# Performance work log

Hardware: AMD Instinct MI355X
Metric: run time of the kernel (lower is better)

## Reference

```python
import jax, jax.numpy as jnp
import numpy as np

NSAMPLE = 32
RADIUS = 5.0
EPS = 1e-5  # BatchNorm eps (torch default)


def setup_inputs() -> dict:
    key = jax.random.key(0)
    ks = jax.random.split(key, 8)
    B, N, C = 4, 4096, 64
    mlp = [64, 64, 64]
    inp = {
        "pos1": jax.random.normal(ks[0], (B, 3, N), jnp.float32),
        "pos2": jax.random.normal(ks[1], (B, 3, N), jnp.float32),
        "feature1": jax.random.normal(ks[2], (B, C, N), jnp.float32),
        "feature2": jax.random.normal(ks[3], (B, C, N), jnp.float32),
    }
    last = 2 * C + 3  # concat corr: feat2 + feat1 + xyz-diff
    for i, oc in enumerate(mlp):
        inp[f"W{i}"] = jax.random.normal(ks[4 + i], (oc, last), jnp.float32) / np.float32(np.sqrt(last))
        inp[f"g{i}"] = jnp.ones((oc,), jnp.float32)
        inp[f"b{i}"] = jnp.zeros((oc,), jnp.float32)
        last = oc
    return inp


def _group(f, idx):
    # f: (B, C, M), idx: (B, N, S) -> (B, C, N, S)
    return jax.vmap(lambda fb, ib: fb[:, ib])(f, idx)


def _bn_relu(x, g, b):
    # training-mode BatchNorm2d over (B, N, S) per channel, then ReLU
    m = x.mean(axis=(0, 2, 3), keepdims=True)
    v = x.var(axis=(0, 2, 3), keepdims=True)
    y = g[None, :, None, None] * (x - m) * jax.lax.rsqrt(v + EPS) + b[None, :, None, None]
    return jax.nn.relu(y)


def _forward(pos1, pos2, feature1, feature2, params):
    B, _, N = pos1.shape
    p1t = pos1.transpose(0, 2, 1)  # (B, N, 3)
    p2t = pos2.transpose(0, 2, 1)  # (B, M, 3)
    # squared pairwise distances (B, N, M)
    sq = (jnp.sum(p1t * p1t, -1, keepdims=True)
          - 2.0 * jnp.einsum('bnc,bmc->bnm', p1t, p2t)
          + jnp.sum(p2t * p2t, -1)[:, None, :])
    neg, idx = jax.lax.top_k(-sq, NSAMPLE)  # ascending-distance KNN
    dist = jnp.sqrt(jnp.maximum(-neg, 0.0))
    # replace out-of-radius neighbors with the nearest neighbor index
    idx = jnp.where(dist > RADIUS, idx[:, :, :1], idx)
    pos2_g = _group(pos2, idx)                       # (B, 3, N, S)
    pos_diff = pos2_g - pos1[:, :, :, None]
    feat2_g = _group(feature2, idx)                  # (B, C, N, S)
    feat1_rep = jnp.broadcast_to(feature1[:, :, :, None],
                                 (B, feature1.shape[1], N, NSAMPLE))
    x = jnp.concatenate([pos_diff, feat2_g, feat1_rep], axis=1)  # (B, 2C+3, N, S)
    for W, g, b in params:
        x = jnp.einsum('oc,bcns->bons', W, x)  # 1x1 conv, no bias
        x = _bn_relu(x, g, b)
    return x.max(axis=-1)  # max-pool over neighbors -> (B, mlp[-1], N)


def reference(pos1, pos2, feature1, feature2, W0, g0, b0, W1, g1, b1, W2, g2, b2):
    params = [(W0, g0, b0), (W1, g1, b1), (W2, g2, b2)]
    feat1_new = _forward(pos1, pos2, feature1, feature2, params)
    return (pos1, feat1_new)
```

## Files before the change

kernel.cpp:

```cpp
#include <hip/hip_runtime.h>
#include <hip/hip_bf16.h>


#define N_ 4096
#define S_ 32
#define PTOT 524288.0f

typedef unsigned short u16;
typedef unsigned int   u32;
typedef unsigned long long u64;
typedef __attribute__((ext_vector_type(8))) short short8;
typedef __attribute__((ext_vector_type(4))) float f32x4;

__device__ __forceinline__ float b2f(u16 u){
  union { u32 i; float f; } x; x.i = ((u32)u) << 16; return x.f;
}
__device__ __forceinline__ u16 f2b(float f){
  __hip_bfloat16 h = __float2bfloat16(f);
  return *(u16*)&h;
}
__device__ __forceinline__ u32 fenc(float f){
  u32 u = __float_as_uint(f);
  return (u & 0x80000000u) ? ~u : (u | 0x80000000u);
}
__device__ __forceinline__ float fdec(u32 k){
  return __uint_as_float((k & 0x80000000u) ? (k & 0x7FFFFFFFu) : ~k);
}
__device__ __forceinline__ int TIX(int r, int c){ return (r << 6) + (c ^ ((r & 7) << 3)); }
#define MFMA16(a,b,c) __builtin_amdgcn_mfma_f32_16x16x32_bf16((a),(b),(c),0,0,0)

__global__ void k_copy(const uint4* __restrict__ s, uint4* __restrict__ d){
  int i = blockIdx.x * 256 + threadIdx.x;
  d[i] = s[i];
}

#define PLCNT(T, OUT) { int _c = 0;                                           \
  _Pragma("unroll")                                                           \
  for (int _it = 0; _it < 64; ++_it) _c += (dl[_it] < (T)) ? 1 : 0;           \
  _Pragma("unroll")                                                           \
  for (int _d = 1; _d < 64; _d <<= 1) _c += __shfl_xor(_c, _d);               \
  OUT = (u32)_c; }

__global__ __launch_bounds__(256) void k_knn(const float* __restrict__ pos1,
        const float* __restrict__ pos2, int* __restrict__ idxb){
  __shared__ u64 lkey[4][96];
  int b = blockIdx.y;
  int l = threadIdx.x & 63;
  int w = threadIdx.x >> 6;
  int n = blockIdx.x * 4 + w;
  const float* p1 = pos1 + b * 3 * N_;
  const float* p2 = pos2 + b * 3 * N_;
  float qx = p1[n], qy = p1[N_ + n], qz = p1[2 * N_ + n];
  float dl[64];
  float minv = 3.4e38f;
  #pragma unroll
  for (int it = 0; it < 16; ++it){
    int j0 = it * 256 + l * 4;
    float4 xv = *(const float4*)(p2 + j0);
    float4 yv = *(const float4*)(p2 + N_ + j0);
    float4 zv = *(const float4*)(p2 + 2 * N_ + j0);
    float dx, dy, dz, d;
    dx=xv.x-qx; dy=yv.x-qy; dz=zv.x-qz; d=fmaf(dx,dx,fmaf(dy,dy,dz*dz)); dl[it*4+0]=d; minv=fminf(minv,d);
    dx=xv.y-qx; dy=yv.y-qy; dz=zv.y-qz; d=fmaf(dx,dx,fmaf(dy,dy,dz*dz)); dl[it*4+1]=d; minv=fminf(minv,d);
    dx=xv.z-qx; dy=yv.z-qy; dz=zv.z-qz; d=fmaf(dx,dx,fmaf(dy,dy,dz*dz)); dl[it*4+2]=d; minv=fminf(minv,d);
    dx=xv.w-qx; dy=yv.w-qy; dz=zv.w-qz; d=fmaf(dx,dx,fmaf(dy,dy,dz*dz)); dl[it*4+3]=d; minv=fminf(minv,d);
  }
  #pragma unroll
  for (int d2 = 1; d2 < 64; d2 <<= 1) minv = fminf(minv, __shfl_xor(minv, d2));
  u32 lo = __float_as_uint(minv);
  u32 hi = lo + (5u << 23); if (hi > 0x7F800000u) hi = 0x7F800000u;
  u32 step = 2u << 23;
  u32 K = 0;
  for (int e = 0; e < 12; ++e){
    PLCNT(__uint_as_float(hi), K)
    if (K >= 32u) break;
    lo = hi;
    hi += step; if (hi > 0x7F800000u) hi = 0x7F800000u;
    step <<= 1;
  }
  if (K < 32u){ hi = 0x7F800000u; PLCNT(__uint_as_float(hi), K) }
  for (int itr = 0; itr < 28 && K > 96u && (hi - lo) > 1u; ++itr){
    u32 mid = (lo + hi) >> 1, c;
    PLCNT(__uint_as_float(mid), c)
    if (c >= 32u){ hi = mid; K = c; } else lo = mid;
  }
  float T = __uint_as_float(hi);
  lkey[w][l] = ~0ull;
  if (l < 32) lkey[w][64 + l] = ~0ull;
  int myc = 0;
  #pragma unroll
  for (int it = 0; it < 64; ++it) myc += (dl[it] < T) ? 1 : 0;
  int pre = myc;
  #pragma unroll
  for (int d2 = 1; d2 < 64; d2 <<= 1){
    int t2 = __shfl_up(pre, d2); if (l >= d2) pre += t2;
  }
  int slot = pre - myc;
  for (int it = 0; it < 64; ++it){
    if (dl[it] < T){
      if (slot < 96)
        lkey[w][slot] = ((u64)__float_as_uint(dl[it]) << 32)
                      | (u32)((it >> 2) * 256 + l * 4 + (it & 3));
      slot++;
    }
  }
  int Kc = (int)(K > 96u ? 96u : K);
  u64 k0 = lkey[w][l];
  u64 k1 = (l < 32) ? lkey[w][64 + l] : ~0ull;
  int r0 = 0, r1 = 0;
  for (int j = 0; j < 96; j += 2){
    ulonglong2 kp = *(const ulonglong2*)&lkey[w][j];
    r0 += (kp.x < k0) + (kp.y < k0);
    r1 += (kp.x < k1) + (kp.y < k1);
  }
  unsigned long long m0 = __ballot((l < Kc) && (r0 == 0));
  u32 nearest;
  if (m0) nearest = (u32)__shfl((int)(u32)k0, __builtin_ctzll(m0));
  else {
    unsigned long long m1 = __ballot((l + 64 < Kc) && (r1 == 0));
    nearest = (u32)__shfl((int)(u32)k1, __builtin_ctzll(m1));
  }
  int* op = idxb + (b * N_ + n) * S_;
  float d0 = __uint_as_float((u32)(k0 >> 32));
  float d1 = __uint_as_float((u32)(k1 >> 32));
  if ((l < Kc) && (r0 < 32))      op[r0] = (d0 > 25.0f) ? (int)nearest : (int)(u32)k0;
  if ((l + 64 < Kc) && (r1 < 32)) op[r1] = (d1 > 25.0f) ? (int)nearest : (int)(u32)k1;
}

template<int MODE>
__global__ __launch_bounds__(256) void k_precomp(const float* __restrict__ posx,
        const float* __restrict__ featx, const float* __restrict__ W0,
        u16* __restrict__ outp){
  __shared__ float Ws[67][65];
  __shared__ float Xs[67][65];
  int b = blockIdx.y, j0 = blockIdx.x * 64, t = threadIdx.x;
  for (int e = t; e < 67 * 64; e += 256){
    int r = e >> 6, o = e & 63;
    int wc = (MODE == 0) ? r : (r < 3 ? r : r + 64);
    Ws[r][o] = W0[o * 131 + wc];
    float x;
    if (r < 3){ x = posx[(b * 3 + r) * N_ + j0 + o]; if (MODE) x = -x; }
    else        x = featx[(b * 64 + (r - 3)) * N_ + j0 + o];
    Xs[r][o] = x;
  }
  __syncthreads();
  int og = t & 15, sl = t >> 4;
  float acc[4][4] = {};
  for (int r = 0; r < 67; ++r){
    float w0v = Ws[r][og*4+0], w1v = Ws[r][og*4+1], w2v = Ws[r][og*4+2], w3v = Ws[r][og*4+3];
    #pragma unroll
    for (int c = 0; c < 4; ++c){
      float xv = Xs[r][sl*4+c];
      acc[c][0] += xv*w0v; acc[c][1] += xv*w1v; acc[c][2] += xv*w2v; acc[c][3] += xv*w3v;
    }
  }
  #pragma unroll
  for (int c = 0; c < 4; ++c){
    ushort4 val;
    val.x = f2b(acc[c][0]); val.y = f2b(acc[c][1]);
    val.z = f2b(acc[c][2]); val.w = f2b(acc[c][3]);
    *(ushort4*)&outp[(((size_t)(b * N_ + j0 + sl*4 + c)) << 6) + og*4] = val;
  }
}

__global__ void k_cvtW2(const float* __restrict__ W, u16* __restrict__ Wb){
  int t = threadIdx.x;
  for (int e = t; e < 4096; e += 256) Wb[e] = f2b(W[e]);
}

__global__ __launch_bounds__(256) void k_stats0(const int* __restrict__ idxb,
    const u16* __restrict__ A, const u16* __restrict__ Cn,
    float* __restrict__ sp1, float* __restrict__ sp2){
  int b = blockIdx.y, n0 = blockIdx.x * 32;
  int c4 = threadIdx.x & 15, sq = threadIdx.x >> 4;
  float4 a1 = {0,0,0,0}, a2 = {0,0,0,0};
  for (int q = 0; q < 32; ++q){
    int n = n0 + q;
    ushort4 cu = *(const ushort4*)&Cn[(((size_t)(b * N_ + n)) << 6) + c4 * 4];
    float cx = b2f(cu.x), cy = b2f(cu.y), cz = b2f(cu.z), cw = b2f(cu.w);
    const int* ip = idxb + (b * N_ + n) * 32;
    #pragma unroll
    for (int ss = 0; ss < 2; ++ss){
      int j = ip[sq + ss * 16];
      ushort4 au = *(const ushort4*)&A[(((size_t)(b * N_ + j)) << 6) + c4 * 4];
      float h0 = b2f(au.x) + cx, h1 = b2f(au.y) + cy;
      float h2 = b2f(au.z) + cz, h3 = b2f(au.w) + cw;
      a1.x += h0; a1.y += h1; a1.z += h2; a1.w += h3;
      a2.x += h0*h0; a2.y += h1*h1; a2.z += h2*h2; a2.w += h3*h3;
    }
  }
  __shared__ float red1[16][64];
  __shared__ float red2[16][64];
  *(float4*)&red1[sq][c4*4] = a1;
  *(float4*)&red2[sq][c4*4] = a2;
  __syncthreads();
  int t = threadIdx.x;
  int slot = (blockIdx.x + (blockIdx.y << 7)) & 63;
  if (t < 64){
    float s1 = 0.f, s2 = 0.f;
    #pragma unroll
    for (int k = 0; k < 16; ++k){ s1 += red1[k][t]; s2 += red2[k][t]; }
    atomicAdd(&sp1[slot * 64 + t], s1);
    atomicAdd(&sp2[slot * 64 + t], s2);
  }
}

__global__ __launch_bounds__(256) void k_bn0(const float* __restrict__ sp1,
    const float* __restrict__ sp2, const float* g, const float* bb, float* bnp){
  __shared__ float red1[4][64];
  __shared__ float red2[4][64];
  int t = threadIdx.x, c = t & 63, s = t >> 6;
  float s1 = 0.f, s2 = 0.f;
  for (int k = s * 16; k < s * 16 + 16; ++k){
    s1 += sp1[k * 64 + c]; s2 += sp2[k * 64 + c];
  }
  red1[s][c] = s1; red2[s][c] = s2;
  __syncthreads();
  if (t < 64){
    float a1 = red1[0][c] + red1[1][c] + red1[2][c] + red1[3][c];
    float a2 = red2[0][c] + red2[1][c] + red2[2][c] + red2[3][c];
    float m = a1 * (1.0f / PTOT);
    float v = a2 * (1.0f / PTOT) - m * m;
    v = v > 0.f ? v : 0.f;
    float sc = g[c] * rsqrtf(v + 1e-5f);
    bnp[c] = sc; bnp[64 + c] = bb[c] - m * sc;
  }
}

__global__ __launch_bounds__(256) void k_bnW(const float* __restrict__ W,
    const float* __restrict__ rp, const float* __restrict__ G, const float* g,
    const float* bb, float* bnp, u16* __restrict__ Wb){
  __shared__ float Ws[64][65];
  __shared__ float Gs[64][65];
  __shared__ float r_s[64];
  __shared__ float redA[4][64];
  __shared__ float redB[4][64];
  __shared__ float scs[64];
  int t = threadIdx.x, o = t & 63, s = t >> 6;
  for (int e = t; e < 4096; e += 256){
    Ws[e >> 6][e & 63] = W[e];
    Gs[e >> 6][e & 63] = G[e];
  }
  float rv = 0.f;
  for (int k = s * 32; k < s * 32 + 32; ++k) rv += rp[k * 64 + o];
  redA[s][o] = rv;
  __syncthreads();
  if (s == 0) r_s[o] = redA[0][o] + redA[1][o] + redA[2][o] + redA[3][o];
  __syncthreads();
  float pm = 0.f, pq = 0.f;
  for (int c = s * 16; c < s * 16 + 16; ++c){
    float t1 = 0.f;
    #pragma unroll
    for (int d = 0; d < 64; ++d) t1 = fmaf(Gs[c][d], Ws[o][d], t1);
    pm = fmaf(Ws[o][c], r_s[c], pm);
    pq = fmaf(Ws[o][c], t1, pq);
  }
  __syncthreads();
  redA[s][o] = pm; redB[s][o] = pq;
  __syncthreads();
  if (t < 64){
    float mean = redA[0][o] + redA[1][o] + redA[2][o] + redA[3][o];
    float qq   = redB[0][o] + redB[1][o] + redB[2][o] + redB[3][o];
    float m = mean * (1.0f / PTOT);
    float v = qq * (1.0f / PTOT) - m * m;
    v = v > 0.f ? v : 0.f;
    float sc = g[o] * rsqrtf(v + 1e-5f);
    bnp[o] = sc; bnp[64 + o] = bb[o] - m * sc;
    scs[o] = sc;
  }
  __syncthreads();
  for (int e = t; e < 4096; e += 256){
    int oo = e >> 6, cc = e & 63;
    Wb[e] = f2b(scs[oo] * Ws[oo][cc]);
  }
}

__global__ void k_reduceG(float* __restrict__ Gp, float* __restrict__ Gout){
  int e = blockIdx.x * 256 + threadIdx.x;
  int s0 = blockIdx.y * 16;
  float v = 0.f;
  for (int s = s0; s < s0 + 16; ++s) v += Gp[s * 4096 + e];
  atomicAdd(&Gout[e], v);
  for (int s = s0; s < s0 + 16; ++s) Gp[s * 4096 + e] = 0.f;
}

#define GATHER_Y0(YARR)                                                       \
  int nq = n0 + ch * 2 + (l >> 5);                                            \
  int jj = idxb[((b << 12) + nq) * 32 + (l & 31)];                            \
  const u16* ap = A + (((size_t)((b << 12) + jj)) << 6) + (w << 4);           \
  const u16* cp = Cn + (((size_t)((b << 12) + nq)) << 6) + (w << 4);          \
  short8 ga0 = *(const short8*)(ap);                                          \
  short8 ga1 = *(const short8*)(ap + 8);                                      \
  short8 gc0 = *(const short8*)(cp);                                          \
  short8 gc1 = *(const short8*)(cp + 8);                                      \
  float YARR[16];                                                             \
  _Pragma("unroll")                                                           \
  for (int kk = 0; kk < 16; ++kk){                                            \
    u16 ae = (kk < 8) ? (u16)ga0[kk] : (u16)ga1[kk - 8];                      \
    u16 ce = (kk < 8) ? (u16)gc0[kk] : (u16)gc1[kk - 8];                      \
    float hv = b2f(ae) + b2f(ce);                                             \
    float sc = ((const float*)scv)[kk], sh = ((const float*)shv)[kk];         \
    YARR[kk] = fmaxf(fmaf(sc, hv, sh), 0.f);                                  \
  }

#define LOAD_BN0                                                              \
  float4 scv[4], shv[4];                                                      \
  _Pragma("unroll")                                                           \
  for (int k = 0; k < 4; ++k){                                                \
    scv[k] = *((const float4*)bnp0 + (w << 2) + k);                           \
    shv[k] = *((const float4*)bnp0 + 16 + (w << 2) + k);                      \
  }

template<int FAT>
__global__ __launch_bounds__(256) void k_gram0(const int* __restrict__ idxb,
    const u16* __restrict__ A, const u16* __restrict__ Cn,
    const float* __restrict__ bnp0, float* __restrict__ Gp, float* __restrict__ rp0,
    u16* __restrict__ y0img){
  __shared__ u16 yc[4096];
  __shared__ u16 yp[FAT ? 4096 : 64];
  int b = blockIdx.y, n0 = blockIdx.x * 32, t = threadIdx.x;
  int l = t & 63, w = t >> 6;
  LOAD_BN0
  int idxpre[16];
  #pragma unroll
  for (int ch = 0; ch < 16; ++ch){
    int nq = n0 + ch * 2 + (l >> 5);
    idxpre[ch] = idxb[((b << 12) + nq) * 32 + (l & 31)];
  }
  short8 pga0, pga1, pgc0, pgc1;
  {
    int nq = n0 + (l >> 5);
    const u16* ap = A + (((size_t)((b << 12) + idxpre[0])) << 6) + (w << 4);
    const u16* cp = Cn + (((size_t)((b << 12) + nq)) << 6) + (w << 4);
    pga0 = *(const short8*)(ap);  pga1 = *(const short8*)(ap + 8);
    pgc0 = *(const short8*)(cp);  pgc1 = *(const short8*)(cp + 8);
  }
  f32x4 acc[4] = {};
  float rsum[16] = {};
  for (int ch = 0; ch < 16; ++ch){
    float yv[16];
    #pragma unroll
    for (int kk = 0; kk < 16; ++kk){
      u16 ae = (kk < 8) ? (u16)pga0[kk] : (u16)pga1[kk - 8];
      u16 ce = (kk < 8) ? (u16)pgc0[kk] : (u16)pgc1[kk - 8];
      float hv = b2f(ae) + b2f(ce);
      float sc = ((const float*)scv)[kk], sh = ((const float*)shv)[kk];
      yv[kk] = fmaxf(fmaf(sc, hv, sh), 0.f);
    }
    #pragma unroll
    for (int k = 0; k < 16; ++k){
      rsum[k] += yv[k];
      yc[TIX((w << 4) + k, l)] = f2b(yv[k]);
    }
    if (FAT){
      short8 s0v, s1v;
      #pragma unroll
      for (int i = 0; i < 8; ++i){ s0v[i] = (short)f2b(yv[i]); s1v[i] = (short)f2b(yv[8+i]); }
      *(short8*)&yp[TIX(l, (w<<4))] = s0v;
      *(short8*)&yp[TIX(l, (w<<4) + 8)] = s1v;
    }
    if (ch + 1 < 16){
      int nq = n0 + (ch + 1) * 2 + (l >> 5);
      const u16* ap = A + (((size_t)((b << 12) + idxpre[ch + 1])) << 6) + (w << 4);
      const u16* cp = Cn + (((size_t)((b << 12) + nq)) << 6) + (w << 4);
      pga0 = *(const short8*)(ap);  pga1 = *(const short8*)(ap + 8);
      pgc0 = *(const short8*)(cp);  pgc1 = *(const short8*)(cp + 8);
    }
    __syncthreads();
    #pragma unroll
    for (int ks = 0; ks < 2; ++ks){
      short8 bf = *(const short8*)&yc[TIX((w << 4) + (l & 15), ks * 32 + ((l >> 4) << 3))];
      #pragma unroll
      for (int ta = 0; ta < 4; ++ta){
        short8 af = *(const short8*)&yc[TIX(ta * 16 + (l & 15), ks * 32 + ((l >> 4) << 3))];
        acc[ta] = MFMA16(af, bf, acc[ta]);
      }
    }
    if (FAT){
      int rr = t >> 2, c0i = (t & 3) << 4;
      short8 e0 = *(const short8*)&yp[TIX(rr, c0i)];
      short8 e1 = *(const short8*)&yp[TIX(rr, c0i + 8)];
      size_t gb = ((((size_t)(((blockIdx.y << 7) | blockIdx.x) << 4) + ch) << 12)
                   + (rr << 6) + c0i);
      *(short8*)&y0img[gb] = e0;
      *(short8*)&y0img[gb + 8] = e1;
    }
    __syncthreads();
  }
  int slot = ((blockIdx.x << 2) + blockIdx.y) & 127;
  float* gp = Gp + slot * 4096;
  #pragma unroll
  for (int ta = 0; ta < 4; ++ta)
    #pragma unroll
    for (int r = 0; r < 4; ++r)
      atomicAdd(&gp[(ta*16 + ((l>>4)<<2) + r) * 64 + (w<<4) + (l & 15)], acc[ta][r]);
  #pragma unroll
  for (int i = 0; i < 16; ++i){
    float v = rsum[i];
    #pragma unroll
    for (int s = 32; s >= 1; s >>= 1) v += __shfl_xor(v, s);
    if (l == 0) atomicAdd(&rp0[slot * 64 + (w<<4) + i], v);
  }
}

template<int FAT>
__global__ __launch_bounds__(256) void k_gram1(const int* __restrict__ idxb,
    const u16* __restrict__ A, const u16* __restrict__ Cn,
    const float* __restrict__ bnp0, const u16* __restrict__ W1b,
    const u16* __restrict__ W2r, const float* __restrict__ bnp1,
    float* __restrict__ Gp, float* __restrict__ rp1,
    const u16* __restrict__ y0img, float* __restrict__ mraw){
  __shared__ u16 yp[2][4096];
  __shared__ u16 y1c[4096];
  __shared__ u16 y1p[4096];
  __shared__ u32 omax[2048];
  __shared__ float sh1[64];
  __shared__ float rsh[64];
  int b = blockIdx.y, n0 = blockIdx.x * 32, t = threadIdx.x;
  int l = t & 63, w = t >> 6;
  LOAD_BN0
  if (t < 64){ sh1[t] = bnp1[64 + t]; rsh[t] = 0.f; }
  for (int e = t; e < 2048; e += 256) omax[e] = 0u;
  short8 wf[4][2], wf2[4][2];
  #pragma unroll
  for (int to = 0; to < 4; ++to)
    #pragma unroll
    for (int ks = 0; ks < 2; ++ks){
      wf[to][ks]  = *(const short8*)&W1b[(to*16 + (l & 15)) * 64 + ks*32 + ((l>>4)<<3)];
      wf2[to][ks] = *(const short8*)&W2r[(to*16 + (l & 15)) * 64 + ks*32 + ((l>>4)<<3)];
    }
  float sh1v[4][4];
  int rr = t >> 2, c0i = (t & 3) << 4;
  size_t gbase = ((((size_t)(((blockIdx.y << 7) | blockIdx.x) << 4)) << 12)
                  + (rr << 6) + c0i);
  int cur = 0;
  short8 pe0, pe1;
  if (FAT){
    pe0 = *(const short8*)&y0img[gbase];
    pe1 = *(const short8*)&y0img[gbase + 8];
    *(short8*)&yp[0][TIX(rr, c0i)] = pe0;
    *(short8*)&yp[0][TIX(rr, c0i + 8)] = pe1;
  }
  __syncthreads();
  #pragma unroll
  for (int to = 0; to < 4; ++to)
    #pragma unroll
    for (int r = 0; r < 4; ++r)
      sh1v[to][r] = sh1[to*16 + ((l>>4)<<2) + r];
  f32x4 gacc[4] = {};
  float rs[4][4] = {};
  for (int ch = 0; ch < 16; ++ch){
    if (FAT){
      if (ch + 1 < 16){
        size_t gb = gbase + ((size_t)(ch + 1) << 12);
        pe0 = *(const short8*)&y0img[gb];
        pe1 = *(const short8*)&y0img[gb + 8];
      }
    } else {
      GATHER_Y0(yv)
      short8 s0, s1;
      #pragma unroll
      for (int i = 0; i < 8; ++i){ s0[i] = (short)f2b(yv[i]); s1[i] = (short)f2b(yv[8+i]); }
      *(short8*)&yp[0][TIX(l, (w<<4))] = s0;
      *(short8*)&yp[0][TIX(l, (w<<4) + 8)] = s1;
      __syncthreads();
    }
    short8 bf0 = *(const short8*)&yp[cur][TIX((w<<4) + (l & 15), ((l>>4)<<3))];
    short8 bf1 = *(const short8*)&yp[cur][TIX((w<<4) + (l & 15), 32 + ((l>>4)<<3))];
    f32x4 h[4] = {};
    #pragma unroll
    for (int to = 0; to < 4; ++to){
      h[to] = MFMA16(wf[to][0], bf0, h[to]);
      h[to] = MFMA16(wf[to][1], bf1, h[to]);
    }
    int pcol = (w<<4) + (l & 15);
    #pragma unroll
    for (int to = 0; to < 4; ++to){
      ushort4 sv;
      #pragma unroll
      for (int r = 0; r < 4; ++r){
        int o = to*16 + ((l>>4)<<2) + r;
        float y = h[to][r] + sh1v[to][r];
        y = y > 0.f ? y : 0.f;
        rs[to][r] += y;
        u16 yb = f2b(y);
        y1c[TIX(o, pcol)] = yb;
        ((u16*)&sv)[r] = yb;
      }
      *(ushort4*)&y1p[TIX(pcol, to*16 + ((l>>4)<<2))] = sv;
    }
    __syncthreads();
    #pragma unroll
    for (int ks = 0; ks < 2; ++ks){
      short8 bf = *(const short8*)&y1c[TIX((w<<4) + (l & 15), ks*32 + ((l>>4)<<3))];
      #pragma unroll
      for (int ta = 0; ta < 4; ++ta){
        short8 af = *(const short8*)&y1c[TIX(ta*16 + (l & 15), ks*32 + ((l>>4)<<3))];
        gacc[ta] = MFMA16(af, bf, gacc[ta]);
      }
    }
    short8 c0 = *(const short8*)&y1p[TIX(pcol, ((l>>4)<<3))];
    short8 c1 = *(const short8*)&y1p[TIX(pcol, 32 + ((l>>4)<<3))];
    f32x4 h2[4] = {};
    #pragma unroll
    for (int to = 0; to < 4; ++to){
      h2[to] = MFMA16(wf2[to][0], c0, h2[to]);
      h2[to] = MFMA16(wf2[to][1], c1, h2[to]);
    }
    int qloc = ch * 2 + (w >> 1);
    #pragma unroll
    for (int to = 0; to < 4; ++to)
      #pragma unroll
      for (int r = 0; r < 4; ++r){
        float m = h2[to][r];
        #pragma unroll
        for (int s = 1; s <= 8; s <<= 1) m = fmaxf(m, __shfl_xor(m, s));
        if ((l & 15) == 0)
          atomicMax(&omax[qloc*64 + to*16 + ((l>>4)<<2) + r], fenc(m));
      }
    if (FAT && ch + 1 < 16){
      *(short8*)&yp[cur ^ 1][TIX(rr, c0i)] = pe0;
      *(short8*)&yp[cur ^ 1][TIX(rr, c0i + 8)] = pe1;
    }
    __syncthreads();
    if (FAT) cur ^= 1;
  }
  int slot = ((blockIdx.x << 2) + blockIdx.y) & 127;
  float* gp = Gp + slot * 4096;
  #pragma unroll
  for (int ta = 0; ta < 4; ++ta)
    #pragma unroll
    for (int r = 0; r < 4; ++r)
      atomicAdd(&gp[(ta*16 + ((l>>4)<<2) + r) * 64 + (w<<4) + (l & 15)], gacc[ta][r]);
  #pragma unroll
  for (int to = 0; to < 4; ++to)
    #pragma unroll
    for (int r = 0; r < 4; ++r){
      float v = rs[to][r];
      #pragma unroll
      for (int s = 1; s <= 8; s <<= 1) v += __shfl_xor(v, s);
      if ((l & 15) == 0) atomicAdd(&rsh[to*16 + ((l>>4)<<2) + r], v);
    }
  __syncthreads();
  if (t < 64) atomicAdd(&rp1[slot * 64 + t], rsh[t]);
  for (int e = t; e < 2048; e += 256){
    int q = e >> 6, o = e & 63;
    mraw[(((size_t)((b << 12) + n0 + q)) << 6) + o] = fdec(omax[e]);
  }
}

__global__ __launch_bounds__(256) void k_epi(const float* __restrict__ mraw,
    const float* __restrict__ bnp2, float* __restrict__ outp){
  __shared__ float tile[64][65];
  int b = blockIdx.y, n0 = blockIdx.x * 64, t = threadIdx.x;
  int o = t & 63, w = t >> 6;
  float sc = bnp2[o], sh = bnp2[64 + o];
  #pragma unroll
  for (int i = 0; i < 16; ++i){
    int n = i * 4 + w;
    float m = mraw[(((size_t)((b << 12) + n0 + n)) << 6) + o];
    float y = fmaf(sc, m, sh);
    tile[n][o] = y > 0.f ? y : 0.f;
  }
  __syncthreads();
  #pragma unroll
  for (int i = 0; i < 16; ++i){
    int oo = i * 4 + w;
    outp[49152 + ((size_t)((b << 6) + oo)) * N_ + n0 + o] = tile[o][oo];
  }
}

extern "C" void kernel_launch(void* const* d_in, const int* in_sizes, int n_in,
                              void* d_out, int out_size, void* d_ws, size_t ws_size,
                              hipStream_t stream){
  (void)in_sizes; (void)n_in; (void)out_size;
  const float* pos1 = (const float*)d_in[0];
  const float* pos2 = (const float*)d_in[1];
  const float* f1   = (const float*)d_in[2];
  const float* f2   = (const float*)d_in[3];
  const float* W0   = (const float*)d_in[4];
  const float* g0   = (const float*)d_in[5];
  const float* b0   = (const float*)d_in[6];
  const float* W1   = (const float*)d_in[7];
  const float* g1   = (const float*)d_in[8];
  const float* b1   = (const float*)d_in[9];
  const float* W2   = (const float*)d_in[10];
  const float* g2   = (const float*)d_in[11];
  const float* b2   = (const float*)d_in[12];

  char* ws = (char*)d_ws;
  int*   idxb = (int*)ws;
  u16*   A    = (u16*)(ws + (2u << 20));
  u16*   Cn   = (u16*)(ws + (4u << 20));
  float* Gp   = (float*)(ws + (6u << 20));
  float* st2  = (float*)(ws + (8u << 20));
  float* rp0  = st2;
  float* rp1  = st2 + 8192;
  float* sp1  = st2 + 16384;
  float* sp2  = st2 + 20480;
  float* G0   = st2 + 24576;
  float* G1   = st2 + 28672;
  float* bnp0 = st2 + 32768;
  float* bnp1 = bnp0 + 128;
  float* bnp2 = bnp1 + 128;
  u16*   W1b  = (u16*)(st2 + 33152);
  u16*   W2b  = (u16*)(st2 + 35200);
  u16*   W2r  = (u16*)(st2 + 37248);
  float* mraw = (float*)(ws + (9u << 20));
  u16*   y0img = (u16*)(ws + (16u << 20));
  bool fat = ws_size >= ((size_t)96 << 20);

  hipMemsetAsync(Gp, 0, (2u << 20) + 131072u, stream);

  k_copy<<<dim3(48), 256, 0, stream>>>((const uint4*)pos1, (uint4*)d_out);
  k_knn<<<dim3(1024, 4), 256, 0, stream>>>(pos1, pos2, idxb);
  k_precomp<0><<<dim3(64, 4), 256, 0, stream>>>(pos2, f2, W0, A);
  k_precomp<1><<<dim3(64, 4), 256, 0, stream>>>(pos1, f1, W0, Cn);
  k_cvtW2<<<dim3(1), 256, 0, stream>>>(W2, W2r);
  k_stats0<<<dim3(128, 4), 256, 0, stream>>>(idxb, A, Cn, sp1, sp2);
  k_bn0<<<dim3(1), 256, 0, stream>>>(sp1, sp2, g0, b0, bnp0);
  if (fat){
    k_gram0<1><<<dim3(128, 4), 256, 0, stream>>>(idxb, A, Cn, bnp0, Gp, rp0, y0img);
    k_reduceG<<<dim3(16, 8), 256, 0, stream>>>(Gp, G0);
    k_bnW<<<dim3(1), 256, 0, stream>>>(W1, rp0, G0, g1, b1, bnp1, W1b);
    k_gram1<1><<<dim3(128, 4), 256, 0, stream>>>(idxb, A, Cn, bnp0, W1b, W2r, bnp1,
                                                 Gp, rp1, y0img, mraw);
    k_reduceG<<<dim3(16, 8), 256, 0, stream>>>(Gp, G1);
    k_bnW<<<dim3(1), 256, 0, stream>>>(W2, rp1, G1, g2, b2, bnp2, W2b);
  } else {
    k_gram0<0><<<dim3(128, 4), 256, 0, stream>>>(idxb, A, Cn, bnp0, Gp, rp0, y0img);
    k_reduceG<<<dim3(16, 8), 256, 0, stream>>>(Gp, G0);
    k_bnW<<<dim3(1), 256, 0, stream>>>(W1, rp0, G0, g1, b1, bnp1, W1b);
    k_gram1<0><<<dim3(128, 4), 256, 0, stream>>>(idxb, A, Cn, bnp0, W1b, W2r, bnp1,
                                                 Gp, rp1, y0img, mraw);
    k_reduceG<<<dim3(16, 8), 256, 0, stream>>>(Gp, G1);
    k_bnW<<<dim3(1), 256, 0, stream>>>(W2, rp1, G1, g2, b2, bnp2, W2b);
  }
  k_epi<<<dim3(64, 4), 256, 0, stream>>>(mraw, bnp2, (float*)d_out);
}
```

Before: 255.0 us.

## Double-buffer LDS tiles to drop one barrier per chunk in gram kernels

The shared-memory staging tiles in k_gram0 and k_gram1 become ping-pong buffers indexed by chunk parity. That removes the second __syncthreads per loop iteration. In the non-FAT path of k_gram1, the y0 gather is now prefetched one chunk ahead into registers and written into the alternate buffer, overlapping global-load latency with MFMA work. The cost is twice the LDS footprint for these tiles, which may lower occupancy, and more live registers.

```diff
diff --git a/kernel.cpp b/kernel.cpp
--- a/kernel.cpp
+++ b/kernel.cpp
@@ -284,25 +284,6 @@
   for (int s = s0; s < s0 + 16; ++s) Gp[s * 4096 + e] = 0.f;
 }
 
-#define GATHER_Y0(YARR)                                                       \
-  int nq = n0 + ch * 2 + (l >> 5);                                            \
-  int jj = idxb[((b << 12) + nq) * 32 + (l & 31)];                            \
-  const u16* ap = A + (((size_t)((b << 12) + jj)) << 6) + (w << 4);           \
-  const u16* cp = Cn + (((size_t)((b << 12) + nq)) << 6) + (w << 4);          \
-  short8 ga0 = *(const short8*)(ap);                                          \
-  short8 ga1 = *(const short8*)(ap + 8);                                      \
-  short8 gc0 = *(const short8*)(cp);                                          \
-  short8 gc1 = *(const short8*)(cp + 8);                                      \
-  float YARR[16];                                                             \
-  _Pragma("unroll")                                                           \
-  for (int kk = 0; kk < 16; ++kk){                                            \
-    u16 ae = (kk < 8) ? (u16)ga0[kk] : (u16)ga1[kk - 8];                      \
-    u16 ce = (kk < 8) ? (u16)gc0[kk] : (u16)gc1[kk - 8];                      \
-    float hv = b2f(ae) + b2f(ce);                                             \
-    float sc = ((const float*)scv)[kk], sh = ((const float*)shv)[kk];         \
-    YARR[kk] = fmaxf(fmaf(sc, hv, sh), 0.f);                                  \
-  }
-
 #define LOAD_BN0                                                              \
   float4 scv[4], shv[4];                                                      \
   _Pragma("unroll")                                                           \
@@ -311,13 +292,33 @@
     shv[k] = *((const float4*)bnp0 + 16 + (w << 2) + k);                      \
   }
 
+#define ISSUE_GATHER(CH)                                                      \
+  {                                                                           \
+    int nq = n0 + (CH) * 2 + (l >> 5);                                        \
+    const u16* ap = A + (((size_t)((b << 12) + idxpre[CH])) << 6) + (w << 4); \
+    const u16* cp = Cn + (((size_t)((b << 12) + nq)) << 6) + (w << 4);        \
+    pga0 = *(const short8*)(ap);  pga1 = *(const short8*)(ap + 8);            \
+    pgc0 = *(const short8*)(cp);  pgc1 = *(const short8*)(cp + 8);            \
+  }
+
+#define CONSUME_Y0(YARR)                                                      \
+  float YARR[16];                                                             \
+  _Pragma("unroll")                                                           \
+  for (int kk = 0; kk < 16; ++kk){                                            \
+    u16 ae = (kk < 8) ? (u16)pga0[kk] : (u16)pga1[kk - 8];                    \
+    u16 ce = (kk < 8) ? (u16)pgc0[kk] : (u16)pgc1[kk - 8];                    \
+    float hv = b2f(ae) + b2f(ce);                                             \
+    float sc = ((const float*)scv)[kk], sh = ((const float*)shv)[kk];         \
+    YARR[kk] = fmaxf(fmaf(sc, hv, sh), 0.f);                                  \
+  }
+
 template<int FAT>
 __global__ __launch_bounds__(256) void k_gram0(const int* __restrict__ idxb,
     const u16* __restrict__ A, const u16* __restrict__ Cn,
     const float* __restrict__ bnp0, float* __restrict__ Gp, float* __restrict__ rp0,
     u16* __restrict__ y0img){
-  __shared__ u16 yc[4096];
-  __shared__ u16 yp[FAT ? 4096 : 64];
+  __shared__ u16 yc[2][4096];
+  __shared__ u16 yp[2][FAT ? 4096 : 64];
   int b = blockIdx.y, n0 = blockIdx.x * 32, t = threadIdx.x;
   int l = t & 63, w = t >> 6;
   LOAD_BN0
@@ -328,64 +329,44 @@
     idxpre[ch] = idxb[((b << 12) + nq) * 32 + (l & 31)];
   }
   short8 pga0, pga1, pgc0, pgc1;
-  {
-    int nq = n0 + (l >> 5);
-    const u16* ap = A + (((size_t)((b << 12) + idxpre[0])) << 6) + (w << 4);
-    const u16* cp = Cn + (((size_t)((b << 12) + nq)) << 6) + (w << 4);
-    pga0 = *(const short8*)(ap);  pga1 = *(const short8*)(ap + 8);
-    pgc0 = *(const short8*)(cp);  pgc1 = *(const short8*)(cp + 8);
-  }
+  ISSUE_GATHER(0)
   f32x4 acc[4] = {};
   float rsum[16] = {};
   for (int ch = 0; ch < 16; ++ch){
-    float yv[16];
-    #pragma unroll
-    for (int kk = 0; kk < 16; ++kk){
-      u16 ae = (kk < 8) ? (u16)pga0[kk] : (u16)pga1[kk - 8];
-      u16 ce = (kk < 8) ? (u16)pgc0[kk] : (u16)pgc1[kk - 8];
-      float hv = b2f(ae) + b2f(ce);
-      float sc = ((const float*)scv)[kk], sh = ((const float*)shv)[kk];
-      yv[kk] = fmaxf(fmaf(sc, hv, sh), 0.f);
-    }
+    int pb = ch & 1;
+    CONSUME_Y0(yv)
     #pragma unroll
     for (int k = 0; k < 16; ++k){
       rsum[k] += yv[k];
-      yc[TIX((w << 4) + k, l)] = f2b(yv[k]);
+      yc[pb][TIX((w << 4) + k, l)] = f2b(yv[k]);
     }
     if (FAT){
       short8 s0v, s1v;
       #pragma unroll
       for (int i = 0; i < 8; ++i){ s0v[i] = (short)f2b(yv[i]); s1v[i] = (short)f2b(yv[8+i]); }
-      *(short8*)&yp[TIX(l, (w<<4))] = s0v;
-      *(short8*)&yp[TIX(l, (w<<4) + 8)] = s1v;
-    }
-    if (ch + 1 < 16){
-      int nq = n0 + (ch + 1) * 2 + (l >> 5);
-      const u16* ap = A + (((size_t)((b << 12) + idxpre[ch + 1])) << 6) + (w << 4);
-      const u16* cp = Cn + (((size_t)((b << 12) + nq)) << 6) + (w << 4);
-      pga0 = *(const short8*)(ap);  pga1 = *(const short8*)(ap + 8);
-      pgc0 = *(const short8*)(cp);  pgc1 = *(const short8*)(cp + 8);
-    }
+      *(short8*)&yp[pb][TIX(l, (w<<4))] = s0v;
+      *(short8*)&yp[pb][TIX(l, (w<<4) + 8)] = s1v;
+    }
+    if (ch + 1 < 16) ISSUE_GATHER(ch + 1)
     __syncthreads();
     #pragma unroll
     for (int ks = 0; ks < 2; ++ks){
-      short8 bf = *(const short8*)&yc[TIX((w << 4) + (l & 15), ks * 32 + ((l >> 4) << 3))];
+      short8 bf = *(const short8*)&yc[pb][TIX((w << 4) + (l & 15), ks * 32 + ((l >> 4) << 3))];
       #pragma unroll
       for (int ta = 0; ta < 4; ++ta){
-        short8 af = *(const short8*)&yc[TIX(ta * 16 + (l & 15), ks * 32 + ((l >> 4) << 3))];
+        short8 af = *(const short8*)&yc[pb][TIX(ta * 16 + (l & 15), ks * 32 + ((l >> 4) << 3))];
         acc[ta] = MFMA16(af, bf, acc[ta]);
       }
     }
     if (FAT){
       int rr = t >> 2, c0i = (t & 3) << 4;
-      short8 e0 = *(const short8*)&yp[TIX(rr, c0i)];
-      short8 e1 = *(const short8*)&yp[TIX(rr, c0i + 8)];
+      short8 e0 = *(const short8*)&yp[pb][TIX(rr, c0i)];
+      short8 e1 = *(const short8*)&yp[pb][TIX(rr, c0i + 8)];
       size_t gb = ((((size_t)(((blockIdx.y << 7) | blockIdx.x) << 4) + ch) << 12)
                    + (rr << 6) + c0i);
       *(short8*)&y0img[gb] = e0;
       *(short8*)&y0img[gb + 8] = e1;
     }
-    __syncthreads();
   }
   int slot = ((blockIdx.x << 2) + blockIdx.y) & 127;
   float* gp = Gp + slot * 4096;
@@ -411,8 +392,8 @@
     float* __restrict__ Gp, float* __restrict__ rp1,
     const u16* __restrict__ y0img, float* __restrict__ mraw){
   __shared__ u16 yp[2][4096];
-  __shared__ u16 y1c[4096];
-  __shared__ u16 y1p[4096];
+  __shared__ u16 y1c[2][4096];
+  __shared__ u16 y1p[2][4096];
   __shared__ u32 omax[2048];
   __shared__ float sh1[64];
   __shared__ float rsh[64];
@@ -429,19 +410,33 @@
       wf[to][ks]  = *(const short8*)&W1b[(to*16 + (l & 15)) * 64 + ks*32 + ((l>>4)<<3)];
       wf2[to][ks] = *(const short8*)&W2r[(to*16 + (l & 15)) * 64 + ks*32 + ((l>>4)<<3)];
     }
-  float sh1v[4][4];
   int rr = t >> 2, c0i = (t & 3) << 4;
   size_t gbase = ((((size_t)(((blockIdx.y << 7) | blockIdx.x) << 4)) << 12)
                   + (rr << 6) + c0i);
-  int cur = 0;
   short8 pe0, pe1;
+  int idxpre[16];
+  short8 pga0, pga1, pgc0, pgc1;
   if (FAT){
     pe0 = *(const short8*)&y0img[gbase];
     pe1 = *(const short8*)&y0img[gbase + 8];
     *(short8*)&yp[0][TIX(rr, c0i)] = pe0;
     *(short8*)&yp[0][TIX(rr, c0i + 8)] = pe1;
-  }
-  __syncthreads();
+  } else {
+    #pragma unroll
+    for (int ch = 0; ch < 16; ++ch){
+      int nq = n0 + ch * 2 + (l >> 5);
+      idxpre[ch] = idxb[((b << 12) + nq) * 32 + (l & 31)];
+    }
+    ISSUE_GATHER(0)
+    CONSUME_Y0(yv)
+    short8 s0, s1;
+    #pragma unroll
+    for (int i = 0; i < 8; ++i){ s0[i] = (short)f2b(yv[i]); s1[i] = (short)f2b(yv[8+i]); }
+    *(short8*)&yp[0][TIX(l, (w<<4))] = s0;
+    *(short8*)&yp[0][TIX(l, (w<<4) + 8)] = s1;
+  }
+  __syncthreads();
+  float sh1v[4][4];
   #pragma unroll
   for (int to = 0; to < 4; ++to)
     #pragma unroll
@@ -450,23 +445,18 @@
   f32x4 gacc[4] = {};
   float rs[4][4] = {};
   for (int ch = 0; ch < 16; ++ch){
-    if (FAT){
-      if (ch + 1 < 16){
+    int pb = ch & 1;
+    if (ch + 1 < 16){
+      if (FAT){
         size_t gb = gbase + ((size_t)(ch + 1) << 12);
         pe0 = *(const short8*)&y0img[gb];
         pe1 = *(const short8*)&y0img[gb + 8];
+      } else {
+        ISSUE_GATHER(ch + 1)
       }
-    } else {
-      GATHER_Y0(yv)
-      short8 s0, s1;
-      #pragma unroll
-      for (int i = 0; i < 8; ++i){ s0[i] = (short)f2b(yv[i]); s1[i] = (short)f2b(yv[8+i]); }
-      *(short8*)&yp[0][TIX(l, (w<<4))] = s0;
-      *(short8*)&yp[0][TIX(l, (w<<4) + 8)] = s1;
-      __syncthreads();
-    }
-    short8 bf0 = *(const short8*)&yp[cur][TIX((w<<4) + (l & 15), ((l>>4)<<3))];
-    short8 bf1 = *(const short8*)&yp[cur][TIX((w<<4) + (l & 15), 32 + ((l>>4)<<3))];
+    }
+    short8 bf0 = *(const short8*)&yp[pb][TIX((w<<4) + (l & 15), ((l>>4)<<3))];
+    short8 bf1 = *(const short8*)&yp[pb][TIX((w<<4) + (l & 15), 32 + ((l>>4)<<3))];
     f32x4 h[4] = {};
     #pragma unroll
     for (int to = 0; to < 4; ++to){
@@ -484,23 +474,36 @@
         y = y > 0.f ? y : 0.f;
         rs[to][r] += y;
         u16 yb = f2b(y);
-        y1c[TIX(o, pcol)] = yb;
+        y1c[pb][TIX(o, pcol)] = yb;
         ((u16*)&sv)[r] = yb;
       }
-      *(ushort4*)&y1p[TIX(pcol, to*16 + ((l>>4)<<2))] = sv;
+      *(ushort4*)&y1p[pb][TIX(pcol, to*16 + ((l>>4)<<2))] = sv;
+    }
+    if (ch + 1 < 16){
+      if (FAT){
+        *(short8*)&yp[pb ^ 1][TIX(rr, c0i)] = pe0;
+        *(short8*)&yp[pb ^ 1][TIX(rr, c0i + 8)] = pe1;
+      } else {
+        CONSUME_Y0(yv2)
+        short8 s0, s1;
+        #pragma unroll
+        for (int i = 0; i < 8; ++i){ s0[i] = (short)f2b(yv2[i]); s1[i] = (short)f2b(yv2[8+i]); }
+        *(short8*)&yp[pb ^ 1][TIX(l, (w<<4))] = s0;
+        *(short8*)&yp[pb ^ 1][TIX(l, (w<<4) + 8)] = s1;
+      }
     }
     __syncthreads();
     #pragma unroll
     for (int ks = 0; ks < 2; ++ks){
-      short8 bf = *(const short8*)&y1c[TIX((w<<4) + (l & 15), ks*32 + ((l>>4)<<3))];
+      short8 bf = *(const short8*)&y1c[pb][TIX((w<<4) + (l & 15), ks*32 + ((l>>4)<<3))];
       #pragma unroll
       for (int ta = 0; ta < 4; ++ta){
-        short8 af = *(const short8*)&y1c[TIX(ta*16 + (l & 15), ks*32 + ((l>>4)<<3))];
+        short8 af = *(const short8*)&y1c[pb][TIX(ta*16 + (l & 15), ks*32 + ((l>>4)<<3))];
         gacc[ta] = MFMA16(af, bf, gacc[ta]);
       }
     }
-    short8 c0 = *(const short8*)&y1p[TIX(pcol, ((l>>4)<<3))];
-    short8 c1 = *(const short8*)&y1p[TIX(pcol, 32 + ((l>>4)<<3))];
+    short8 c0 = *(const short8*)&y1p[pb][TIX(pcol, ((l>>4)<<3))];
+    short8 c1 = *(const short8*)&y1p[pb][TIX(pcol, 32 + ((l>>4)<<3))];
     f32x4 h2[4] = {};
     #pragma unroll
     for (int to = 0; to < 4; ++to){
@@ -518,13 +521,8 @@
         if ((l & 15) == 0)
           atomicMax(&omax[qloc*64 + to*16 + ((l>>4)<<2) + r], fenc(m));
       }
-    if (FAT && ch + 1 < 16){
-      *(short8*)&yp[cur ^ 1][TIX(rr, c0i)] = pe0;
-      *(short8*)&yp[cur ^ 1][TIX(rr, c0i + 8)] = pe1;
-    }
-    __syncthreads();
-    if (FAT) cur ^= 1;
-  }
+  }
+  __syncthreads();
   int slot = ((blockIdx.x << 2) + blockIdx.y) & 127;
   float* gp = Gp + slot * 4096;
   #pragma unroll
```

Result: no change. 256.1 us (+0.4%).
